# Kernel tuning notes

Hardware: AMD Instinct MI355X
Metric: run time of the kernel (lower is better)

## Reference

```python
import jax, jax.numpy as jnp
import numpy as np

EPS = 1e-7  # keras _EPSILON

def _boost_generators():
    # Standard symmetric Lorentz boost generators K_x, K_y, K_z (4x4, metric (t,x,y,z))
    Kg = np.zeros((3, 4, 4), dtype=np.float32)
    for i in range(3):
        Kg[i, 0, i + 1] = 1.0
        Kg[i, i + 1, 0] = 1.0
    return jnp.asarray(Kg)


def setup_inputs() -> dict:
    key = jax.random.key(0)
    k1, k2 = jax.random.split(key)
    # T: (batch, cluster, 4) input 4-vectors
    T = jax.random.normal(k1, (8192, 1024, 4), dtype=jnp.float32)
    # Bo: learned per-cluster Cartesian boost 3-vectors, init uniform*0.33 as in build()
    Bo = jax.random.uniform(k2, (1024, 3), dtype=jnp.float32) * 0.33
    return {"T": T, "Bo": Bo}


def reference(T, Bo):
    Kg = _boost_generators()                     # (3,4,4)
    x = T[:, :, 0:4]                             # vec_start = 0
    # per-cluster boost magnitude / direction / gamma
    mag = jnp.clip(jnp.sqrt(jnp.sum(jnp.square(Bo), axis=1, keepdims=True)), EPS, 1.0 - EPS)  # (C,1)
    n = Bo / mag                                 # (C,3) unit directions
    g = 1.0 / jnp.sqrt(1.0 - jnp.square(mag))    # (C,1) Lorentz gamma
    # n . K : per-cluster 4x4 generator contraction
    nK = jnp.einsum('ci,ijk->cjk', n, Kg)        # (C,4,4)
    nK2 = jnp.einsum('cij,cjk->cik', nK, nK)     # (C,4,4)
    I4 = jnp.eye(4, dtype=T.dtype)
    # B = I - (gamma*beta)(n.K) + (gamma-1)(n.K)^2
    B = I4 - (g * mag)[:, :, None] * nK + (g - 1.0)[:, :, None] * nK2  # (C,4,4)
    # apply per-cluster boost to every batch element: out[b,c,i] = B[c,i,j] x[b,c,j]
    return jnp.einsum('cij,bcj->bci', B, x)
```

## Files before the change

### kernel.cpp

```cpp
#include <hip/hip_runtime.h>

#define EPS 1e-7f

typedef float fx4 __attribute__((ext_vector_type(4)));

__global__ __launch_bounds__(256) void lorentz_params_kernel(
    const float* __restrict__ Bo, fx4* __restrict__ P, int C)
{
    int c = blockIdx.x * blockDim.x + threadIdx.x;
    if (c >= C) return;
    float b0 = Bo[c * 3 + 0];
    float b1 = Bo[c * 3 + 1];
    float b2 = Bo[c * 3 + 2];
    float mag = sqrtf(b0 * b0 + b1 * b1 + b2 * b2);
    mag = fminf(fmaxf(mag, EPS), 1.0f - EPS);
    float inv = 1.0f / mag;
    float n0 = b0 * inv, n1 = b1 * inv, n2 = b2 * inv;
    float g = 1.0f / sqrtf(1.0f - mag * mag);
    float nn = n0 * n0 + n1 * n1 + n2 * n2;
    float B00 = 1.0f + (g - 1.0f) * nn;
    fx4 pa = {n0, n1, n2, B00};
    fx4 pb = {g * mag, g - 1.0f, 0.0f, 0.0f};
    P[c * 2 + 0] = pa;
    P[c * 2 + 1] = pb;
}

__global__ __launch_bounds__(256) void lorentz_apply_kernel(
    const fx4* __restrict__ T, const fx4* __restrict__ P,
    fx4* __restrict__ out, int total)
{
    int idx = blockIdx.x * blockDim.x + threadIdx.x;
    if (idx >= total) return;
    int c = idx & 1023;

    fx4 x  = __builtin_nontemporal_load(&T[idx]);
    fx4 pa = P[c * 2 + 0];
    fx4 pb = P[c * 2 + 1];

    float d  = pa.x * x.y + pa.y * x.z + pa.z * x.w;
    float o0 = pa.w * x.x - pb.x * d;
    float s  = pb.y * d - pb.x * x.x;
    fx4 o = {o0,
             x.y + pa.x * s,
             x.z + pa.y * s,
             x.w + pa.z * s};
    __builtin_nontemporal_store(o, &out[idx]);
}

extern "C" void kernel_launch(void* const* d_in, const int* in_sizes, int n_in,
                              void* d_out, int out_size, void* d_ws, size_t ws_size,
                              hipStream_t stream)
{
    const fx4* T  = (const fx4*)d_in[0];
    const float* Bo = (const float*)d_in[1];
    fx4* out = (fx4*)d_out;
    fx4* P   = (fx4*)d_ws;

    int C = in_sizes[1] / 3;
    int total = out_size / 4;

    lorentz_params_kernel<<<(C + 255) / 256, 256, 0, stream>>>(Bo, P, C);
    lorentz_apply_kernel<<<(total + 255) / 256, 256, 0, stream>>>(T, P, out, total);
}
```

Measured before the change: 221.4 us.

## Fuse boost-parameter computation into apply kernel with 4-way strided unroll

Merges the per-cluster parameter kernel into the apply kernel, so each thread recomputes its cluster's boost parameters from Bo and then applies them to four grid-strided elements. The grid is rounded so the stride is a multiple of C and the cluster index stays constant across a thread's four elements. This removes a kernel launch and the workspace round-trip, and amortizes the sqrt/div math over four loads issued up front. It assumes C is a power of two (cmask = C-1), and the rounded grid may leave some threads idle.

```diff
diff --git a/kernel.cpp b/kernel.cpp
--- a/kernel.cpp
+++ b/kernel.cpp
@@ -4,11 +4,14 @@
 
 typedef float fx4 __attribute__((ext_vector_type(4)));
 
-__global__ __launch_bounds__(256) void lorentz_params_kernel(
-    const float* __restrict__ Bo, fx4* __restrict__ P, int C)
+__global__ __launch_bounds__(256) void lorentz_fused_kernel(
+    const fx4* __restrict__ T, const float* __restrict__ Bo,
+    fx4* __restrict__ out, int total, int cmask)
 {
-    int c = blockIdx.x * blockDim.x + threadIdx.x;
-    if (c >= C) return;
+    const int S = gridDim.x * blockDim.x;
+    const int idx = blockIdx.x * blockDim.x + threadIdx.x;
+    const int c = idx & cmask;
+
     float b0 = Bo[c * 3 + 0];
     float b1 = Bo[c * 3 + 1];
     float b2 = Bo[c * 3 + 2];
@@ -19,32 +22,38 @@
     float g = 1.0f / sqrtf(1.0f - mag * mag);
     float nn = n0 * n0 + n1 * n1 + n2 * n2;
     float B00 = 1.0f + (g - 1.0f) * nn;
-    fx4 pa = {n0, n1, n2, B00};
-    fx4 pb = {g * mag, g - 1.0f, 0.0f, 0.0f};
-    P[c * 2 + 0] = pa;
-    P[c * 2 + 1] = pb;
-}
+    float gm = g * mag;
+    float gm1 = g - 1.0f;
 
-__global__ __launch_bounds__(256) void lorentz_apply_kernel(
-    const fx4* __restrict__ T, const fx4* __restrict__ P,
-    fx4* __restrict__ out, int total)
-{
-    int idx = blockIdx.x * blockDim.x + threadIdx.x;
-    if (idx >= total) return;
-    int c = idx & 1023;
+    fx4 x0v, x1v, x2v, x3v;
+    const int i0 = idx;
+    const int i1 = idx + S;
+    const int i2 = idx + 2 * S;
+    const int i3 = idx + 3 * S;
+    if (i0 < total) x0v = __builtin_nontemporal_load(&T[i0]);
+    if (i1 < total) x1v = __builtin_nontemporal_load(&T[i1]);
+    if (i2 < total) x2v = __builtin_nontemporal_load(&T[i2]);
+    if (i3 < total) x3v = __builtin_nontemporal_load(&T[i3]);
 
-    fx4 x  = __builtin_nontemporal_load(&T[idx]);
-    fx4 pa = P[c * 2 + 0];
-    fx4 pb = P[c * 2 + 1];
+#define APPLY_STORE(xv, ii)                                        \
+    do {                                                           \
+        if ((ii) < total) {                                        \
+            fx4 v = (xv);                                          \
+            float d = n0 * v.y + n1 * v.z + n2 * v.w;              \
+            float s = gm1 * d - gm * v.x;                          \
+            fx4 o = {B00 * v.x - gm * d,                           \
+                     v.y + n0 * s,                                 \
+                     v.z + n1 * s,                                 \
+                     v.w + n2 * s};                                \
+            __builtin_nontemporal_store(o, &out[ii]);              \
+        }                                                          \
+    } while (0)
 
-    float d  = pa.x * x.y + pa.y * x.z + pa.z * x.w;
-    float o0 = pa.w * x.x - pb.x * d;
-    float s  = pb.y * d - pb.x * x.x;
-    fx4 o = {o0,
-             x.y + pa.x * s,
-             x.z + pa.y * s,
-             x.w + pa.z * s};
-    __builtin_nontemporal_store(o, &out[idx]);
+    APPLY_STORE(x0v, i0);
+    APPLY_STORE(x1v, i1);
+    APPLY_STORE(x2v, i2);
+    APPLY_STORE(x3v, i3);
+#undef APPLY_STORE
 }
 
 extern "C" void kernel_launch(void* const* d_in, const int* in_sizes, int n_in,
@@ -54,11 +63,15 @@
     const fx4* T  = (const fx4*)d_in[0];
     const float* Bo = (const float*)d_in[1];
     fx4* out = (fx4*)d_out;
-    fx4* P   = (fx4*)d_ws;
 
-    int C = in_sizes[1] / 3;
-    int total = out_size / 4;
+    const int C = in_sizes[1] / 3;
+    const int total = out_size / 4;
 
-    lorentz_params_kernel<<<(C + 255) / 256, 256, 0, stream>>>(Bo, P, C);
-    lorentz_apply_kernel<<<(total + 255) / 256, 256, 0, stream>>>(T, P, out, total);
+    const int UNROLL = 4;
+    const int BLOCK = 256;
+    int blocks = (total + BLOCK * UNROLL - 1) / (BLOCK * UNROLL);
+    const int align = (C + BLOCK - 1) / BLOCK;
+    blocks = ((blocks + align - 1) / align) * align;
+
+    lorentz_fused_kernel<<<blocks, BLOCK, 0, stream>>>(T, Bo, out, total, C - 1);
 }
```

Measured after the change: 226.3 us. +2.2%, slower.
